# Kernel tuning notes

Hardware: AMD Instinct MI355X
Metric: run time of the kernel (lower is better)

Reference implementation:

```python
import jax, jax.numpy as jnp
import numpy as np

N = 100000      # nodes
E = 1600000     # edges
G = 64          # graphs in batch
H = 128         # hidden (== num_features)
L = 4           # num_layers
C = 16          # num_classes
NCAND = 100000  # candidate edges
BN_EPS = 1e-5


def setup_inputs() -> dict:
    key = jax.random.key(0)
    ks = jax.random.split(key, 24)
    s = 0.05
    inp = {}
    inp["x"] = jax.random.normal(ks[0], (N, H), dtype=jnp.float32)
    inp["edge_index"] = jax.random.randint(ks[1], (2, E), 0, N)
    inp["batch"] = jnp.sort(jax.random.randint(ks[2], (N,), 0, G))
    inp["candidate_edges"] = jax.random.randint(ks[3], (2, NCAND), 0, N)
    # GIN conv params, stacked over L layers (all layers are H->H since num_features==hidden)
    inp["cW1"] = jax.random.normal(ks[4], (L, H, H), dtype=jnp.float32) * s
    inp["cb1"] = jnp.zeros((L, H), jnp.float32)
    inp["cW2"] = jax.random.normal(ks[5], (L, H, H), dtype=jnp.float32) * s
    inp["cb2"] = jnp.zeros((L, H), jnp.float32)
    inp["cgamma"] = jnp.ones((L, H), jnp.float32)
    inp["cbeta"] = jnp.zeros((L, H), jnp.float32)
    inp["ceps"] = jnp.zeros((L,), jnp.float32)  # train_eps=True, init 0
    # node classifier: L*H -> 2H -> H -> H -> C (dropout is identity in eval)
    inp["ncW1"] = jax.random.normal(ks[6], (L * H, 2 * H), dtype=jnp.float32) * s
    inp["ncb1"] = jnp.zeros((2 * H,), jnp.float32)
    inp["ncW2"] = jax.random.normal(ks[7], (2 * H, H), dtype=jnp.float32) * s
    inp["ncb2"] = jnp.zeros((H,), jnp.float32)
    inp["ncW3"] = jax.random.normal(ks[8], (H, H), dtype=jnp.float32) * s
    inp["ncb3"] = jnp.zeros((H,), jnp.float32)
    inp["ncW4"] = jax.random.normal(ks[9], (H, C), dtype=jnp.float32) * s
    inp["ncb4"] = jnp.zeros((C,), jnp.float32)
    # edge predictor: 2*L*H -> 2H -> H -> 1
    inp["epW1"] = jax.random.normal(ks[10], (2 * L * H, 2 * H), dtype=jnp.float32) * s
    inp["epb1"] = jnp.zeros((2 * H,), jnp.float32)
    inp["epW2"] = jax.random.normal(ks[11], (2 * H, H), dtype=jnp.float32) * s
    inp["epb2"] = jnp.zeros((H,), jnp.float32)
    inp["epW3"] = jax.random.normal(ks[12], (H, 1), dtype=jnp.float32) * s
    inp["epb3"] = jnp.zeros((1,), jnp.float32)
    return inp


def _forward(x, cW1, cb1, cW2, cb2, cgamma, cbeta, ceps,
             ncW1, ncb1, ncW2, ncb2, ncW3, ncb3, ncW4, ncb4,
             epW1, epb1, epW2, epb2, epW3, epb3,
             edge_index, batch, candidate_edges):
    src, dst = edge_index[0], edge_index[1]
    h = x
    xs = []
    for l in range(L):
        # GIN: (1+eps)*x_i + sum_{j->i} x_j  (scatter-add over destination nodes)
        agg = jax.ops.segment_sum(h[src], dst, num_segments=N)
        z = (1.0 + ceps[l]) * h + agg
        z = jax.nn.relu(z @ cW1[l] + cb1[l])
        z = jax.nn.relu(z @ cW2[l] + cb2[l])
        # BatchNorm1d (training-mode batch statistics, biased variance)
        mu = z.mean(axis=0)
        var = jnp.var(z, axis=0)
        h = (z - mu) * jax.lax.rsqrt(var + BN_EPS) * cgamma[l] + cbeta[l]
        xs.append(h)
    emb = jnp.concatenate(xs, axis=-1)  # [N, L*H]
    # global mean pool over graphs
    sums = jax.ops.segment_sum(emb, batch, num_segments=G)
    cnt = jax.ops.segment_sum(jnp.ones((N, 1), emb.dtype), batch, num_segments=G)
    gemb = sums / jnp.maximum(cnt, 1.0)  # [G, L*H]
    t = jax.nn.relu(gemb @ ncW1 + ncb1)
    t = jax.nn.relu(t @ ncW2 + ncb2)
    t = jax.nn.relu(t @ ncW3 + ncb3)
    class_output = jax.nn.log_softmax(t @ ncW4 + ncb4, axis=1)  # [G, C]
    # link prediction: gather node embeddings per candidate edge
    ef = jnp.concatenate([emb[candidate_edges[0]], emb[candidate_edges[1]]], axis=1)  # [NC, 2*L*H]
    u = jax.nn.relu(ef @ epW1 + epb1)
    u = jax.nn.relu(u @ epW2 + epb2)
    edge_scores = jax.nn.sigmoid((u @ epW3 + epb3).squeeze(-1))  # [NC]
    return class_output, edge_scores


def reference(x, cW1, cb1, cW2, cb2, cgamma, cbeta, ceps,
              ncW1, ncb1, ncW2, ncb2, ncW3, ncb3, ncW4, ncb4,
              epW1, epb1, epW2, epb2, epW3, epb3,
              edge_index, batch, candidate_edges):
    return _forward(x, cW1, cb1, cW2, cb2, cgamma, cbeta, ceps,
                    ncW1, ncb1, ncW2, ncb2, ncW3, ncb3, ncW4, ncb4,
                    epW1, epb1, epW2, epb2, epW3, epb3,
                    edge_index, batch, candidate_edges)
```

## Files before the change

### kernel.cpp

```cpp
#include <hip/hip_runtime.h>
#include <math.h>

#define NN 100000
#define EE 1600000
#define GG 64
#define HH 128
#define LL 4
#define CCLS 16
#define NC 100000
#define NB 49
#define LDK 40
#define LDA2 136
#define LDC 260

typedef __attribute__((ext_vector_type(8))) short bf16x8;
typedef __attribute__((ext_vector_type(4))) float f32x4;

__device__ __forceinline__ unsigned short f2bf(float x) {
  union { float f; unsigned int u; } v; v.f = x;
  unsigned int r = v.u + 0x7fffu + ((v.u >> 16) & 1u);
  return (unsigned short)(r >> 16);
}
__device__ __forceinline__ float bl(unsigned u) {
  union { unsigned u; float f; } v; v.u = u << 16; return v.f;
}
__device__ __forceinline__ float bh(unsigned u) {
  union { unsigned u; float f; } v; v.u = u & 0xffff0000u; return v.f;
}

__global__ void hist_kernel(const int* __restrict__ dst, int* __restrict__ cnt, int E) {
  int i = (blockIdx.x * 256 + threadIdx.x) * 4;
  if (i + 3 < E) {
    int4 v = *(const int4*)(dst + i);
    atomicAdd(&cnt[v.x], 1);
    atomicAdd(&cnt[v.y], 1);
    atomicAdd(&cnt[v.z], 1);
    atomicAdd(&cnt[v.w], 1);
  } else {
    for (int k = i; k < E; ++k) atomicAdd(&cnt[dst[k]], 1);
  }
}

__global__ __launch_bounds__(256) void scan_p1(const int* __restrict__ cnt,
                                               int* __restrict__ bsum, int n) {
  __shared__ int red[256];
  int tid = threadIdx.x;
  int base = blockIdx.x * 1024 + tid * 4;
  int s = 0;
  if (base + 3 < n) {
    int4 v = *(const int4*)(cnt + base);
    s = v.x + v.y + v.z + v.w;
  } else {
    for (int i = 0; i < 4; ++i) if (base + i < n) s += cnt[base + i];
  }
  red[tid] = s;
  __syncthreads();
  for (int st = 128; st >= 1; st >>= 1) {
    if (tid < st) red[tid] += red[tid + st];
    __syncthreads();
  }
  if (tid == 0) bsum[blockIdx.x] = red[0];
}

__global__ void scan_p2(int* __restrict__ bsum, int* __restrict__ rowptr,
                        int* __restrict__ bcursor, int nb, int n) {
  __shared__ int buf[128];
  int tid = threadIdx.x;
  int v = (tid < nb) ? bsum[tid] : 0;
  buf[tid] = v;
  __syncthreads();
  for (int off = 1; off < 128; off <<= 1) {
    int t = (tid >= off) ? buf[tid - off] : 0;
    __syncthreads();
    buf[tid] += t;
    __syncthreads();
  }
  if (tid < nb) bsum[tid] = buf[tid] - v;
  if (tid == 127) rowptr[n] = buf[127];
  __syncthreads();
  if (tid < NB) bcursor[tid] = bsum[2 * tid];
}

__global__ __launch_bounds__(256) void scan_p3(const int* __restrict__ cnt,
                                               const int* __restrict__ bsum,
                                               int* __restrict__ rowptr,
                                               int* __restrict__ cursor, int n) {
  __shared__ int red[256];
  int tid = threadIdx.x;
  int base = blockIdx.x * 1024 + tid * 4;
  int v[4] = {0, 0, 0, 0};
  if (base + 3 < n) {
    int4 t = *(const int4*)(cnt + base);
    v[0] = t.x; v[1] = t.y; v[2] = t.z; v[3] = t.w;
  } else {
    for (int i = 0; i < 4; ++i) if (base + i < n) v[i] = cnt[base + i];
  }
  int s = v[0] + v[1] + v[2] + v[3];
  red[tid] = s;
  __syncthreads();
  for (int off = 1; off < 256; off <<= 1) {
    int t = (tid >= off) ? red[tid - off] : 0;
    __syncthreads();
    red[tid] += t;
    __syncthreads();
  }
  int run = bsum[blockIdx.x] + red[tid] - s;
  int4 o;
  o.x = run; o.y = run + v[0]; o.z = o.y + v[1]; o.w = o.z + v[2];
  if (base + 3 < n) {
    *(int4*)(rowptr + base) = o;
    *(int4*)(cursor + base) = o;
  } else {
    int oo[4] = {o.x, o.y, o.z, o.w};
    for (int i = 0; i < 4; ++i)
      if (base + i < n) { rowptr[base + i] = oo[i]; cursor[base + i] = oo[i]; }
  }
}

__global__ __launch_bounds__(256) void partition_kernel(const int* __restrict__ src,
                                                        const int* __restrict__ dst,
                                                        int* __restrict__ bcursor,
                                                        int2* __restrict__ pairs, int E) {
  __shared__ int sS[4096];
  __shared__ int sD[4096];
  __shared__ int hist[NB];
  __shared__ int base[NB];
  int tid = threadIdx.x;
  int base_e = blockIdx.x * 4096;
  int cnt = min(4096, E - base_e);
  if (tid < NB) hist[tid] = 0;
  for (int i = tid * 4; i < cnt; i += 1024) {
    if (i + 3 < cnt) {
      *(int4*)(sS + i) = *(const int4*)(src + base_e + i);
      *(int4*)(sD + i) = *(const int4*)(dst + base_e + i);
    } else {
      for (int k = i; k < cnt; ++k) { sS[k] = src[base_e + k]; sD[k] = dst[base_e + k]; }
    }
  }
  __syncthreads();
  for (int i = tid; i < cnt; i += 256) atomicAdd(&hist[sD[i] >> 11], 1);
  __syncthreads();
  if (tid < NB) {
    base[tid] = atomicAdd(&bcursor[tid], hist[tid]);
    hist[tid] = 0;
  }
  __syncthreads();
  for (int i = tid; i < cnt; i += 256) {
    int d = sD[i];
    int b = d >> 11;
    int off = atomicAdd(&hist[b], 1);
    pairs[base[b] + off] = make_int2(sS[i], d);
  }
}

__global__ __launch_bounds__(256) void scatter_csr(const int2* __restrict__ pairs,
                                                   const int* __restrict__ rowptr,
                                                   int* __restrict__ cursor,
                                                   int* __restrict__ csr_src) {
  int b = blockIdx.x % NB;
  int slice = blockIdx.x / NB;
  int start = rowptr[b * 2048];
  int endn = min((b + 1) * 2048, NN);
  int end = rowptr[endn];
  for (int i = start + slice * 256 + threadIdx.x; i < end; i += 8 * 256) {
    int2 p = pairs[i];
    int pos = atomicAdd(&cursor[p.y], 1);
    csr_src[pos] = p.x;
  }
}

#define NF2B (NN * HH / 4)
#define NCVW (LL * 16384 + 32768)
__global__ void convert_all(const float* __restrict__ x, unsigned short* __restrict__ x16,
                            const float* __restrict__ cW1, const float* __restrict__ cW2,
                            unsigned short* __restrict__ WT1, unsigned short* __restrict__ WT2,
                            const float* __restrict__ epW2, unsigned short* __restrict__ W2T) {
  int gi = blockIdx.x * 256 + threadIdx.x;
  if (gi < NF2B) {
    float4 v = ((const float4*)x)[gi];
    unsigned short r[4] = {f2bf(v.x), f2bf(v.y), f2bf(v.z), f2bf(v.w)};
    *(uint2*)(x16 + (size_t)gi * 4) = *(uint2*)r;
    return;
  }
  int idx = gi - NF2B;
  if (idx < LL * 16384) {
    int l = idx >> 14, r = idx & 16383, k = r >> 7, n = r & 127;
    WT1[l * 16384 + n * 128 + k] = f2bf(cW1[idx]);
    WT2[l * 16384 + n * 128 + k] = f2bf(cW2[idx]);
  } else if (idx < NCVW) {
    int j = idx - LL * 16384;
    int k = j >> 7, n = j & 127;
    W2T[(size_t)n * 256 + k] = f2bf(epW2[j]);
  }
}

__global__ __launch_bounds__(256) void ep_w1_prep(
    const float* __restrict__ epW1, const float* __restrict__ epb1,
    const float* __restrict__ bnsum, const float* __restrict__ bnsumsq,
    const float* __restrict__ gamma, const float* __restrict__ beta,
    unsigned short* __restrict__ W1T, float* __restrict__ b1x) {
  __shared__ float red[256];
  int n = blockIdx.x;
  int tid = threadIdx.x;
  const float inv_n = 1.0f / (float)NN;
  int k0 = tid * 4;
  unsigned short w16[4];
  float part = 0.f;
#pragma unroll
  for (int j = 0; j < 4; ++j) {
    int k = k0 + j;
    int c = k & 511;
    float mu = bnsum[c] * inv_n;
    float var = bnsumsq[c] * inv_n - mu * mu;
    float s = rsqrtf(var + 1e-5f) * gamma[c];
    float o = beta[c] - s * mu;
    float w = epW1[(size_t)k * 256 + n];
    w16[j] = f2bf(s * w);
    part += o * w;
  }
  *(uint2*)(W1T + (size_t)n * 1024 + k0) = *(uint2*)w16;
  red[tid] = part;
  __syncthreads();
  for (int st = 128; st >= 1; st >>= 1) {
    if (tid < st) red[tid] += red[tid + st];
    __syncthreads();
  }
  if (tid == 0) b1x[n] = epb1[n] + red[0];
}

__global__ __launch_bounds__(256, 8) void aggregate_bf16(
    const unsigned short* __restrict__ h16, int ld,
    const int* __restrict__ rowptr,
    const int* __restrict__ csr_src,
    const float* __restrict__ ceps_l,
    const float* __restrict__ bnsum_prev,
    const float* __restrict__ bnsumsq_prev,
    const float* __restrict__ gamma_prev,
    const float* __restrict__ beta_prev,
    unsigned short* __restrict__ out, int n) {
  int wave = threadIdx.x >> 6;
  int lane = threadIdx.x & 63;
  int sub = lane >> 4;
  int li = lane & 15;
  int node = blockIdx.x * 16 + wave * 4 + sub;
  if (node >= n) return;
  int c8 = li * 8;
  float acc[8] = {};
  int b = rowptr[node], e = rowptr[node + 1];
  int j = b;
  for (; j + 4 <= e; j += 4) {
    uint4 u[4];
#pragma unroll
    for (int t = 0; t < 4; ++t) {
      int s = csr_src[j + t];
      u[t] = *(const uint4*)(h16 + (size_t)s * ld + c8);
    }
#pragma unroll
    for (int t = 0; t < 4; ++t) {
      acc[0] += bl(u[t].x); acc[1] += bh(u[t].x);
      acc[2] += bl(u[t].y); acc[3] += bh(u[t].y);
      acc[4] += bl(u[t].z); acc[5] += bh(u[t].z);
      acc[6] += bl(u[t].w); acc[7] += bh(u[t].w);
    }
  }
  for (; j < e; ++j) {
    int s = csr_src[j];
    uint4 u = *(const uint4*)(h16 + (size_t)s * ld + c8);
    acc[0] += bl(u.x); acc[1] += bh(u.x);
    acc[2] += bl(u.y); acc[3] += bh(u.y);
    acc[4] += bl(u.z); acc[5] += bh(u.z);
    acc[6] += bl(u.w); acc[7] += bh(u.w);
  }
  float eps1 = 1.0f + *ceps_l;
  uint4 hu = *(const uint4*)(h16 + (size_t)node * ld + c8);
  acc[0] = fmaf(eps1, bl(hu.x), acc[0]); acc[1] = fmaf(eps1, bh(hu.x), acc[1]);
  acc[2] = fmaf(eps1, bl(hu.y), acc[2]); acc[3] = fmaf(eps1, bh(hu.y), acc[3]);
  acc[4] = fmaf(eps1, bl(hu.z), acc[4]); acc[5] = fmaf(eps1, bh(hu.z), acc[5]);
  acc[6] = fmaf(eps1, bl(hu.w), acc[6]); acc[7] = fmaf(eps1, bh(hu.w), acc[7]);
  float degw = (float)(e - b) + eps1;
  unsigned short o[8];
  if (bnsum_prev) {
    const float inv_n = 1.0f / (float)NN;
#pragma unroll
    for (int k = 0; k < 8; ++k) {
      int c = c8 + k;
      float mu = bnsum_prev[c] * inv_n;
      float var = bnsumsq_prev[c] * inv_n - mu * mu;
      float s = rsqrtf(var + 1e-5f) * gamma_prev[c];
      float off = beta_prev[c] - s * mu;
      o[k] = f2bf(fmaf(s, acc[k], degw * off));
    }
  } else {
#pragma unroll
    for (int k = 0; k < 8; ++k) o[k] = f2bf(acc[k]);
  }
  *(uint4*)(out + (size_t)node * 128 + c8) = *(uint4*)o;
}

__global__ __launch_bounds__(256) void trunk_fused(
    const unsigned short* __restrict__ A16,
    const unsigned short* __restrict__ W1T, const float* __restrict__ b1,
    const unsigned short* __restrict__ W2T, const float* __restrict__ b2,
    float* __restrict__ bnsum, float* __restrict__ bnsumsq,
    unsigned short* __restrict__ C16 , int M) {
  __shared__ unsigned short As[128 * LDA2];
  __shared__ unsigned short Bs[128 * LDA2];
  const int tid = threadIdx.x;
  const int bm = blockIdx.x * 128;
  const int lane = tid & 63;
  const int wave = tid >> 6;
  const int wr = (wave >> 1) << 6;
  const int wc = (wave & 1) << 6;
  const int ar = tid >> 1;
  const int ah = (tid & 1) << 4;
  int gra = bm + ar; if (gra >= M) gra = M - 1;
  const unsigned short* Arow = A16 + (size_t)gra * 128;
  const unsigned short* B1row = W1T + (size_t)ar * 128;
  const int mrow = lane & 15;
  const int kq = (lane >> 4) << 3;

  {
    uint4 aR[8], bR[8];
#pragma unroll
    for (int i = 0; i < 4; ++i) {
      aR[2 * i]     = *(const uint4*)(Arow + (i << 5) + ah);
      aR[2 * i + 1] = *(const uint4*)(Arow + (i << 5) + ah + 8);
      bR[2 * i]     = *(const uint4*)(B1row + (i << 5) + ah);
      bR[2 * i + 1] = *(const uint4*)(B1row + (i << 5) + ah + 8);
    }
#pragma unroll
    for (int i = 0; i < 4; ++i) {
      *(uint4*)(As + ar * LDA2 + (i << 5) + ah)     = aR[2 * i];
      *(uint4*)(As + ar * LDA2 + (i << 5) + ah + 8) = aR[2 * i + 1];
      *(uint4*)(Bs + ar * LDA2 + (i << 5) + ah)     = bR[2 * i];
      *(uint4*)(Bs + ar * LDA2 + (i << 5) + ah + 8) = bR[2 * i + 1];
    }
  }
  f32x4 acc[4][4] = {};
  __syncthreads();
#pragma unroll
  for (int ks = 0; ks < 4; ++ks) {
    const int k0 = ks << 5;
    bf16x8 af[4], bfv[4];
#pragma unroll
    for (int t = 0; t < 4; ++t)
      af[t] = *(const bf16x8*)(As + (wr + t * 16 + mrow) * LDA2 + k0 + kq);
#pragma unroll
    for (int t = 0; t < 4; ++t)
      bfv[t] = *(const bf16x8*)(Bs + (wc + t * 16 + mrow) * LDA2 + k0 + kq);
#pragma unroll
    for (int mt = 0; mt < 4; ++mt)
#pragma unroll
      for (int nt = 0; nt < 4; ++nt)
        acc[mt][nt] = __builtin_amdgcn_mfma_f32_16x16x32_bf16(af[mt], bfv[nt], acc[mt][nt], 0, 0, 0);
  }
  uint4 w2[8];
  {
    const unsigned short* B2row = W2T + (size_t)ar * 128;
#pragma unroll
    for (int i = 0; i < 4; ++i) {
      w2[2 * i]     = *(const uint4*)(B2row + (i << 5) + ah);
      w2[2 * i + 1] = *(const uint4*)(B2row + (i << 5) + ah + 8);
    }
  }
  __syncthreads();
  const int crow = (lane >> 4) << 2;
  const int ccol = lane & 15;
#pragma unroll
  for (int nt = 0; nt < 4; ++nt) {
    int c = wc + nt * 16 + ccol;
    float bz = b1[c];
#pragma unroll
    for (int mt = 0; mt < 4; ++mt) {
      int rl = wr + mt * 16 + crow;
#pragma unroll
      for (int i = 0; i < 4; ++i)
        As[(rl + i) * LDA2 + c] = f2bf(fmaxf(acc[mt][nt][i] + bz, 0.f));
    }
  }
#pragma unroll
  for (int i = 0; i < 4; ++i) {
    *(uint4*)(Bs + ar * LDA2 + (i << 5) + ah)     = w2[2 * i];
    *(uint4*)(Bs + ar * LDA2 + (i << 5) + ah + 8) = w2[2 * i + 1];
  }
#pragma unroll
  for (int mt = 0; mt < 4; ++mt)
#pragma unroll
    for (int nt = 0; nt < 4; ++nt)
      acc[mt][nt] = (f32x4){0.f, 0.f, 0.f, 0.f};
  __syncthreads();
#pragma unroll
  for (int ks = 0; ks < 4; ++ks) {
    const int k0 = ks << 5;
    bf16x8 af[4], bfv[4];
#pragma unroll
    for (int t = 0; t < 4; ++t)
      af[t] = *(const bf16x8*)(As + (wr + t * 16 + mrow) * LDA2 + k0 + kq);
#pragma unroll
    for (int t = 0; t < 4; ++t)
      bfv[t] = *(const bf16x8*)(Bs + (wc + t * 16 + mrow) * LDA2 + k0 + kq);
#pragma unroll
    for (int mt = 0; mt < 4; ++mt)
#pragma unroll
      for (int nt = 0; nt < 4; ++nt)
        acc[mt][nt] = __builtin_amdgcn_mfma_f32_16x16x32_bf16(af[mt], bfv[nt], acc[mt][nt], 0, 0, 0);
  }
  __syncthreads();
#pragma unroll
  for (int nt = 0; nt < 4; ++nt) {
    int c = wc + nt * 16 + ccol;
    float bz = b2[c];
    float s = 0.f, q = 0.f;
#pragma unroll
    for (int mt = 0; mt < 4; ++mt) {
      int rl = wr + mt * 16 + crow;
      int rbase = bm + rl;
#pragma unroll
      for (int i = 0; i < 4; ++i) {
        float v = fmaxf(acc[mt][nt][i] + bz, 0.f);
        Bs[(rl + i) * LDA2 + c] = f2bf(v);
        if (rbase + i < M) { s += v; q += v * v; }
      }
    }
    s += __shfl_xor(s, 16, 64);
    s += __shfl_xor(s, 32, 64);
    q += __shfl_xor(q, 16, 64);
    q += __shfl_xor(q, 32, 64);
    if (lane < 16) {
      atomicAdd(&bnsum[c], s);
      atomicAdd(&bnsumsq[c], q);
    }
  }
  __syncthreads();
#pragma unroll
  for (int p = 0; p < 8; ++p) {
    int r = p * 16 + (tid >> 4);
    int q8 = (tid & 15) * 8;
    if (bm + r < M)
      *(uint4*)(C16 + (size_t)(bm + r) * 512 + q8) =
          *(const uint4*)(Bs + r * LDA2 + q8);
  }
}

__global__ __launch_bounds__(512, 4) void ep_fused(
    const unsigned short* __restrict__ emb16, const int* __restrict__ cand,
    const unsigned short* __restrict__ W1T ,
    const float* __restrict__ b1,
    const unsigned short* __restrict__ W2T ,
    const float* __restrict__ b2, const float* __restrict__ epW3,
    const float* __restrict__ epb3,
    float* __restrict__ out, int M) {
  __shared__ unsigned short smem[128 * LDC];
  __shared__ float sDotA[128];
  __shared__ float sDotB[128];
  unsigned short* const As0 = smem;
  unsigned short* const As1 = smem + 128 * LDK;
  unsigned short* const Bs0 = smem + 2 * 128 * LDK;
  unsigned short* const Bs1 = smem + 2 * 128 * LDK + 256 * LDK;
  const int tid = threadIdx.x;
  const int bm = blockIdx.x * 128;
  const int lane = tid & 63;
  const int wave = tid >> 6;
  const int wr = (wave >> 2) << 6;
  const int wc = (wave & 3) << 6;
  f32x4 acc[4][4] = {};
  const int ar = tid >> 2;
  const int ah = (tid & 3) << 3;
  int gra = bm + ar; if (gra >= M) gra = M - 1;
  const int node0 = cand[gra];
  const int node1 = cand[NC + gra];
  const int br = tid >> 1;
  const int bh8 = (tid & 1) << 4;
  const unsigned short* Brow = W1T + (size_t)br * 1024 + bh8;
  const unsigned short* Arow0 = emb16 + (size_t)node0 * 512 + ah;
  const unsigned short* Arow1 = emb16 + (size_t)node1 * 512 + ah - 512;
  const int mrow = lane & 15;
  const int kq = (lane >> 4) << 3;

  auto ldA = [&](int k) -> uint4 {
    const unsigned short* p = (k < 16) ? Arow0 : Arow1;
    return *(const uint4*)(p + (k << 5));
  };
  auto ldB0v = [&](int k) -> uint4 { return *(const uint4*)(Brow + (k << 5)); };
  auto ldB1v = [&](int k) -> uint4 { return *(const uint4*)(Brow + (k << 5) + 8); };
  auto stTile = [&](unsigned short* Ab, unsigned short* Bb, uint4 a, uint4 x0, uint4 x1) {
    *(uint4*)(Ab + ar * LDK + ah) = a;
    *(uint4*)(Bb + br * LDK + bh8) = x0;
    *(uint4*)(Bb + br * LDK + bh8 + 8) = x1;
  };
  auto mma_step = [&](const unsigned short* A, const unsigned short* B) {
    bf16x8 af[4], bfv[4];
#pragma unroll
    for (int t = 0; t < 4; ++t)
      af[t] = *(const bf16x8*)(A + (wr + t * 16 + mrow) * LDK + kq);
#pragma unroll
    for (int t = 0; t < 4; ++t)
      bfv[t] = *(const bf16x8*)(B + (wc + t * 16 + mrow) * LDK + kq);
#pragma unroll
    for (int mt = 0; mt < 4; ++mt)
#pragma unroll
      for (int nt = 0; nt < 4; ++nt)
        acc[mt][nt] = __builtin_amdgcn_mfma_f32_16x16x32_bf16(af[mt], bfv[nt], acc[mt][nt], 0, 0, 0);
  };

  uint4 aA, aB, b0, b1v;
  {
    uint4 a0 = ldA(0), x0 = ldB0v(0), x1 = ldB1v(0);
    stTile(As0, Bs0, a0, x0, x1);
    aA = ldA(1); b0 = ldB0v(1); b1v = ldB1v(1);
    aB = ldA(2);
  }
  __syncthreads();
  for (int it = 0; it < 16; ++it) {
    const int s0 = 2 * it;
    stTile(As1, Bs1, aA, b0, b1v);
    if (s0 + 3 < 32) aA = ldA(s0 + 3);
    if (s0 + 2 < 32) { b0 = ldB0v(s0 + 2); b1v = ldB1v(s0 + 2); }
    mma_step(As0, Bs0);
    __syncthreads();
    const int s1 = s0 + 1;
    if (s1 < 31) {
      stTile(As0, Bs0, aB, b0, b1v);
      if (s1 + 3 < 32) aB = ldA(s1 + 3);
      if (s1 + 2 < 32) { b0 = ldB0v(s1 + 2); b1v = ldB1v(s1 + 2); }
    }
    mma_step(As1, Bs1);
    __syncthreads();
  }

  const int crow = (lane >> 4) << 2;
  const int ccol = lane & 15;
#pragma unroll
  for (int nt = 0; nt < 4; ++nt) {
    int c = wc + nt * 16 + ccol;
    float bz = b1[c];
#pragma unroll
    for (int mt = 0; mt < 4; ++mt) {
      int rl = wr + mt * 16 + crow;
#pragma unroll
      for (int i = 0; i < 4; ++i)
        smem[(rl + i) * LDC + c] = f2bf(fmaxf(acc[mt][nt][i] + bz, 0.f));
    }
  }
  __syncthreads();
  const int wr2 = (wave >> 1) << 5;
  const int wc2 = (wave & 1) << 6;
  f32x4 acc2[2][4] = {};
  for (int ks = 0; ks < 8; ++ks) {
    const int k0 = ks << 5;
    bf16x8 af[2], bfv[4];
#pragma unroll
    for (int t = 0; t < 2; ++t)
      af[t] = *(const bf16x8*)(smem + (wr2 + t * 16 + mrow) * LDC + k0 + kq);
#pragma unroll
    for (int t = 0; t < 4; ++t)
      bfv[t] = *(const bf16x8*)(W2T + (size_t)(wc2 + t * 16 + mrow) * 256 + k0 + kq);
#pragma unroll
    for (int mt = 0; mt < 2; ++mt)
#pragma unroll
      for (int nt = 0; nt < 4; ++nt)
        acc2[mt][nt] = __builtin_amdgcn_mfma_f32_16x16x32_bf16(af[mt], bfv[nt], acc2[mt][nt], 0, 0, 0);
  }
  float w3v[4], bz2[4];
#pragma unroll
  for (int nt = 0; nt < 4; ++nt) {
    int c = wc2 + nt * 16 + ccol;
    w3v[nt] = epW3[c];
    bz2[nt] = b2[c];
  }
  float* sBank = (wave & 1) ? sDotB : sDotA;
#pragma unroll
  for (int mt = 0; mt < 2; ++mt) {
#pragma unroll
    for (int i = 0; i < 4; ++i) {
      int rl = wr2 + mt * 16 + crow + i;
      float p = 0.f;
#pragma unroll
      for (int nt = 0; nt < 4; ++nt)
        p = fmaf(fmaxf(acc2[mt][nt][i] + bz2[nt], 0.f), w3v[nt], p);
      p += __shfl_xor(p, 1, 64);
      p += __shfl_xor(p, 2, 64);
      p += __shfl_xor(p, 4, 64);
      p += __shfl_xor(p, 8, 64);
      if ((lane & 15) == 0) sBank[rl] = p;
    }
  }
  __syncthreads();
  if (tid < 128) {
    int r = bm + tid;
    if (r < M) out[r] = 1.f / (1.f + expf(-(sDotA[tid] + sDotB[tid] + epb3[0])));
  }
}

__global__ __launch_bounds__(256) void pool_bf16(const unsigned short* __restrict__ emb16,
                                                 const int* __restrict__ batch,
                                                 float* __restrict__ gsum) {
  __shared__ int se[2];
  __shared__ float sRed[512];
  int g = blockIdx.x;
  int chunk = blockIdx.y;
  int tid = threadIdx.x;
  if (tid < 2) {
    int x = g + tid;
    int lo = 0, hi = NN;
    while (lo < hi) {
      int mid = (lo + hi) >> 1;
      if (batch[mid] < x) lo = mid + 1; else hi = mid;
    }
    se[tid] = lo;
  }
  __syncthreads();
  int s = se[0], e = se[1];
  int len = e - s;
  int per = (len + 7) >> 3;
  int r0 = s + chunk * per;
  int r1 = min(r0 + per, e);
  int c8 = (tid & 63) * 8;
  int wgrp = tid >> 6;
  float acc[8] = {};
  for (int r = r0 + wgrp; r < r1; r += 4) {
    uint4 u = *(const uint4*)(emb16 + (size_t)r * 512 + c8);
    acc[0] += bl(u.x); acc[1] += bh(u.x);
    acc[2] += bl(u.y); acc[3] += bh(u.y);
    acc[4] += bl(u.z); acc[5] += bh(u.z);
    acc[6] += bl(u.w); acc[7] += bh(u.w);
  }
  if (wgrp == 0) {
#pragma unroll
    for (int j = 0; j < 8; ++j) sRed[c8 + j] = acc[j];
  }
  __syncthreads();
  for (int w = 1; w < 4; ++w) {
    if (wgrp == w) {
#pragma unroll
      for (int j = 0; j < 8; ++j) sRed[c8 + j] += acc[j];
    }
    __syncthreads();
  }
  if (r0 < r1 && tid < 128) {
#pragma unroll
    for (int j = 0; j < 4; ++j)
      atomicAdd(&gsum[g * 512 + tid * 4 + j], sRed[tid * 4 + j]);
  }
}

__global__ __launch_bounds__(256) void nc_fused(
    const float* __restrict__ gsum, const int* __restrict__ batch,
    const float* __restrict__ bnsum, const float* __restrict__ bnsumsq,
    const float* __restrict__ gamma, const float* __restrict__ beta,
    const float* __restrict__ W1, const float* __restrict__ b1,
    const float* __restrict__ W2, const float* __restrict__ b2,
    const float* __restrict__ W3, const float* __restrict__ b3,
    const float* __restrict__ W4, const float* __restrict__ b4,
    float* __restrict__ out) {
  __shared__ float row[512];
  __shared__ float t1[256];
  __shared__ float t2[128];
  __shared__ float t3s[128];
  __shared__ float lg[16];
  __shared__ int se[2];
  int g = blockIdx.x;
  int tid = threadIdx.x;
  if (tid < 2) {
    int x = g + tid;
    int lo = 0, hi = NN;
    while (lo < hi) {
      int mid = (lo + hi) >> 1;
      if (batch[mid] < x) lo = mid + 1; else hi = mid;
    }
    se[tid] = lo;
  }
  __syncthreads();
  float inv = 1.0f / fmaxf((float)(se[1] - se[0]), 1.0f);
  const float inv_n = 1.0f / (float)NN;
#pragma unroll
  for (int h = 0; h < 2; ++h) {
    int c = tid + h * 256;
    float mu = bnsum[c] * inv_n;
    float var = bnsumsq[c] * inv_n - mu * mu;
    float s = rsqrtf(var + 1e-5f) * gamma[c];
    float o = beta[c] - s * mu;
    row[c] = fmaf(gsum[g * 512 + c] * inv, s, o);
  }
  __syncthreads();
  {
    float acc = b1[tid];
#pragma unroll 8
    for (int k = 0; k < 512; ++k) acc = fmaf(row[k], W1[k * 256 + tid], acc);
    t1[tid] = fmaxf(acc, 0.f);
  }
  __syncthreads();
  if (tid < 128) {
    float acc = b2[tid];
#pragma unroll 8
    for (int k = 0; k < 256; ++k) acc = fmaf(t1[k], W2[k * 128 + tid], acc);
    t2[tid] = fmaxf(acc, 0.f);
  }
  __syncthreads();
  if (tid < 128) {
    float acc = b3[tid];
#pragma unroll 8
    for (int k = 0; k < 128; ++k) acc = fmaf(t2[k], W3[k * 128 + tid], acc);
    t3s[tid] = fmaxf(acc, 0.f);
  }
  __syncthreads();
  if (tid < 16) {
    float acc = b4[tid];
#pragma unroll 8
    for (int k = 0; k < 128; ++k) acc = fmaf(t3s[k], W4[k * 16 + tid], acc);
    lg[tid] = acc;
  }
  __syncthreads();
  if (tid < 16) {
    float v = lg[tid];
    float m = v;
    for (int j = 0; j < 16; ++j) m = fmaxf(m, lg[j]);
    float s = 0.f;
    for (int j = 0; j < 16; ++j) s += expf(lg[j] - m);
    out[g * 16 + tid] = v - m - logf(s);
  }
}

extern "C" void kernel_launch(void* const* d_in, const int* in_sizes, int n_in,
                              void* d_out, int out_size, void* d_ws, size_t ws_size,
                              hipStream_t stream) {
  const float* x = (const float*)d_in[0];
  const int* edge_index = (const int*)d_in[1];
  const int* batch = (const int*)d_in[2];
  const int* cand = (const int*)d_in[3];
  const float* cW1 = (const float*)d_in[4];
  const float* cb1 = (const float*)d_in[5];
  const float* cW2 = (const float*)d_in[6];
  const float* cb2 = (const float*)d_in[7];
  const float* cgamma = (const float*)d_in[8];
  const float* cbeta = (const float*)d_in[9];
  const float* ceps = (const float*)d_in[10];
  const float* ncW1 = (const float*)d_in[11];
  const float* ncb1 = (const float*)d_in[12];
  const float* ncW2 = (const float*)d_in[13];
  const float* ncb2 = (const float*)d_in[14];
  const float* ncW3 = (const float*)d_in[15];
  const float* ncb3 = (const float*)d_in[16];
  const float* ncW4 = (const float*)d_in[17];
  const float* ncb4 = (const float*)d_in[18];
  const float* epW1 = (const float*)d_in[19];
  const float* epb1 = (const float*)d_in[20];
  const float* epW2 = (const float*)d_in[21];
  const float* epb2 = (const float*)d_in[22];
  const float* epW3 = (const float*)d_in[23];
  const float* epb3 = (const float*)d_in[24];

  char* ws = (char*)d_ws;
  size_t off = 0;
  auto alloc = [&](size_t bytes) -> void* {
    off = (off + 255) & ~(size_t)255;
    void* p = ws + off;
    off += bytes;
    return p;
  };
  size_t zz_bytes = (size_t)NN * 4 + 512 * 4 + 512 * 4 + (size_t)GG * 512 * 4;
  char* zz = (char*)alloc(zz_bytes);
  int* cnt = (int*)zz;
  float* bnsum = (float*)(zz + (size_t)NN * 4);
  float* bnsumsq = bnsum + 512;
  float* gsum = bnsumsq + 512;
  int* rowptr = (int*)alloc((size_t)(NN + 1) * 4);
  int* cursor = (int*)alloc((size_t)NN * 4);
  int* csr_src = (int*)alloc((size_t)EE * 4);
  int2* pairs = (int2*)alloc((size_t)EE * 8);
  int* bsum = (int*)alloc(128 * 4);
  int* bcursor = (int*)alloc(64 * 4);
  unsigned short* x16 = (unsigned short*)alloc((size_t)NN * 128 * 2);
  unsigned short* g16a = (unsigned short*)alloc((size_t)NN * 128 * 2);
  unsigned short* emb16 = (unsigned short*)alloc((size_t)NN * 512 * 2);
  unsigned short* WT1 = (unsigned short*)alloc((size_t)LL * 16384 * 2);
  unsigned short* WT2 = (unsigned short*)alloc((size_t)LL * 16384 * 2);
  unsigned short* W1T = (unsigned short*)alloc((size_t)1024 * 256 * 2);
  unsigned short* W2T = (unsigned short*)alloc((size_t)256 * 128 * 2);
  float* b1x = (float*)alloc(256 * 4);

  const int* esrc = edge_index;
  const int* edst = edge_index + EE;
  const int nblk = (NN + 1023) / 1024;
  const int nech = (EE + 4095) / 4096;

  hipMemsetAsync(zz, 0, zz_bytes, stream);
  hist_kernel<<<(EE / 4 + 255) / 256, 256, 0, stream>>>(edst, cnt, EE);
  scan_p1<<<nblk, 256, 0, stream>>>(cnt, bsum, NN);
  scan_p2<<<1, 128, 0, stream>>>(bsum, rowptr, bcursor, nblk, NN);
  scan_p3<<<nblk, 256, 0, stream>>>(cnt, bsum, rowptr, cursor, NN);
  partition_kernel<<<nech, 256, 0, stream>>>(esrc, edst, bcursor, pairs, EE);
  scatter_csr<<<NB * 8, 256, 0, stream>>>(pairs, rowptr, cursor, csr_src);
  convert_all<<<(NF2B + NCVW + 255) / 256, 256, 0, stream>>>(
      x, x16, cW1, cW2, WT1, WT2, epW2, W2T);

  for (int l = 0; l < LL; ++l) {
    const unsigned short* h16 = (l == 0) ? x16 : (emb16 + (size_t)(l - 1) * 128);
    int ld = (l == 0) ? 128 : 512;
    aggregate_bf16<<<(NN + 15) / 16, 256, 0, stream>>>(
        h16, ld, rowptr, csr_src, ceps + l,
        (l == 0) ? nullptr : bnsum + (l - 1) * 128,
        (l == 0) ? nullptr : bnsumsq + (l - 1) * 128,
        (l == 0) ? nullptr : cgamma + (l - 1) * 128,
        (l == 0) ? nullptr : cbeta + (l - 1) * 128,
        g16a, NN);
    trunk_fused<<<(NN + 127) / 128, 256, 0, stream>>>(
        g16a, WT1 + (size_t)l * 16384, cb1 + l * 128,
        WT2 + (size_t)l * 16384, cb2 + l * 128,
        bnsum + l * 128, bnsumsq + l * 128, emb16 + (size_t)l * 128, NN);
  }
  ep_w1_prep<<<256, 256, 0, stream>>>(epW1, epb1, bnsum, bnsumsq, cgamma, cbeta,
                                      W1T, b1x);

  pool_bf16<<<dim3(GG, 8), 256, 0, stream>>>(emb16, batch, gsum);
  nc_fused<<<GG, 256, 0, stream>>>(gsum, batch, bnsum, bnsumsq, cgamma, cbeta,
                                   ncW1, ncb1, ncW2, ncb2, ncW3, ncb3,
                                   ncW4, ncb4, (float*)d_out);

  ep_fused<<<(NC + 127) / 128, 512, 0, stream>>>(
      emb16, cand, W1T, b1x, W2T, epb2, epW3, epb3,
      (float*)d_out + GG * CCLS, NC);
}
```

Baseline: 1.002 ms.

## Use finer 256-node buckets and LDS-local sort to build CSR

Edge partitioning now uses 391 buckets of 256 destination nodes instead of 49 buckets of 2048, and the CSR scatter sorts each bucket inside shared memory with per-node offsets in LDS. Each bucket's sorted sources are then written back contiguously. This removes the global cursor array and the global atomics with scattered writes in the final CSR pass. In exchange there are more buckets, so more global atomics on bcursor per partition block, plus a fallback path when a bucket exceeds the shared-memory capacity.

```diff
diff --git a/kernel.cpp b/kernel.cpp
--- a/kernel.cpp
+++ b/kernel.cpp
@@ -8,7 +8,8 @@
 #define LL 4
 #define CCLS 16
 #define NC 100000
-#define NB 49
+#define NB2 391
+#define SCAP 6144
 #define LDK 40
 #define LDA2 136
 #define LDC 260
@@ -62,8 +63,7 @@
   if (tid == 0) bsum[blockIdx.x] = red[0];
 }
 
-__global__ void scan_p2(int* __restrict__ bsum, int* __restrict__ rowptr,
-                        int* __restrict__ bcursor, int nb, int n) {
+__global__ void scan_p2(int* __restrict__ bsum, int* __restrict__ rowptr, int nb, int n) {
   __shared__ int buf[128];
   int tid = threadIdx.x;
   int v = (tid < nb) ? bsum[tid] : 0;
@@ -77,14 +77,11 @@
   }
   if (tid < nb) bsum[tid] = buf[tid] - v;
   if (tid == 127) rowptr[n] = buf[127];
-  __syncthreads();
-  if (tid < NB) bcursor[tid] = bsum[2 * tid];
 }
 
 __global__ __launch_bounds__(256) void scan_p3(const int* __restrict__ cnt,
                                                const int* __restrict__ bsum,
-                                               int* __restrict__ rowptr,
-                                               int* __restrict__ cursor, int n) {
+                                               int* __restrict__ rowptr, int n) {
   __shared__ int red[256];
   int tid = threadIdx.x;
   int base = blockIdx.x * 1024 + tid * 4;
@@ -109,12 +106,16 @@
   o.x = run; o.y = run + v[0]; o.z = o.y + v[1]; o.w = o.z + v[2];
   if (base + 3 < n) {
     *(int4*)(rowptr + base) = o;
-    *(int4*)(cursor + base) = o;
   } else {
     int oo[4] = {o.x, o.y, o.z, o.w};
     for (int i = 0; i < 4; ++i)
-      if (base + i < n) { rowptr[base + i] = oo[i]; cursor[base + i] = oo[i]; }
-  }
+      if (base + i < n) rowptr[base + i] = oo[i];
+  }
+}
+
+__global__ void bcursor_init(const int* __restrict__ rowptr, int* __restrict__ bcursor) {
+  int b = blockIdx.x * 256 + threadIdx.x;
+  if (b < NB2) bcursor[b] = rowptr[b * 256];
 }
 
 __global__ __launch_bounds__(256) void partition_kernel(const int* __restrict__ src,
@@ -123,12 +124,12 @@
                                                         int2* __restrict__ pairs, int E) {
   __shared__ int sS[4096];
   __shared__ int sD[4096];
-  __shared__ int hist[NB];
-  __shared__ int base[NB];
+  __shared__ int hist[NB2 + 1];
+  __shared__ int base[NB2 + 1];
   int tid = threadIdx.x;
   int base_e = blockIdx.x * 4096;
   int cnt = min(4096, E - base_e);
-  if (tid < NB) hist[tid] = 0;
+  for (int h = tid; h < NB2; h += 256) hist[h] = 0;
   for (int i = tid * 4; i < cnt; i += 1024) {
     if (i + 3 < cnt) {
       *(int4*)(sS + i) = *(const int4*)(src + base_e + i);
@@ -138,34 +139,48 @@
     }
   }
   __syncthreads();
-  for (int i = tid; i < cnt; i += 256) atomicAdd(&hist[sD[i] >> 11], 1);
-  __syncthreads();
-  if (tid < NB) {
-    base[tid] = atomicAdd(&bcursor[tid], hist[tid]);
-    hist[tid] = 0;
+  for (int i = tid; i < cnt; i += 256) atomicAdd(&hist[sD[i] >> 8], 1);
+  __syncthreads();
+  for (int h = tid; h < NB2; h += 256) {
+    base[h] = atomicAdd(&bcursor[h], hist[h]);
+    hist[h] = 0;
   }
   __syncthreads();
   for (int i = tid; i < cnt; i += 256) {
     int d = sD[i];
-    int b = d >> 11;
+    int b = d >> 8;
     int off = atomicAdd(&hist[b], 1);
     pairs[base[b] + off] = make_int2(sS[i], d);
   }
 }
 
-__global__ __launch_bounds__(256) void scatter_csr(const int2* __restrict__ pairs,
-                                                   const int* __restrict__ rowptr,
-                                                   int* __restrict__ cursor,
-                                                   int* __restrict__ csr_src) {
-  int b = blockIdx.x % NB;
-  int slice = blockIdx.x / NB;
-  int start = rowptr[b * 2048];
-  int endn = min((b + 1) * 2048, NN);
-  int end = rowptr[endn];
-  for (int i = start + slice * 256 + threadIdx.x; i < end; i += 8 * 256) {
-    int2 p = pairs[i];
-    int pos = atomicAdd(&cursor[p.y], 1);
-    csr_src[pos] = p.x;
+__global__ __launch_bounds__(256) void scatter_sort(const int2* __restrict__ pairs,
+                                                    const int* __restrict__ rowptr,
+                                                    int* __restrict__ csr_src) {
+  __shared__ int lofs[256];
+  __shared__ int sbuf[SCAP];
+  int b = blockIdx.x;
+  int tid = threadIdx.x;
+  int n0 = b * 256;
+  int nodes = min(256, NN - n0);
+  int pstart = rowptr[n0];
+  int L = rowptr[n0 + nodes] - pstart;
+  if (tid < nodes) lofs[tid] = rowptr[n0 + tid] - pstart;
+  __syncthreads();
+  if (L <= SCAP) {
+    for (int i = tid; i < L; i += 256) {
+      int2 p = pairs[pstart + i];
+      int pos = atomicAdd(&lofs[p.y - n0], 1);
+      sbuf[pos] = p.x;
+    }
+    __syncthreads();
+    for (int i = tid; i < L; i += 256) csr_src[pstart + i] = sbuf[i];
+  } else {
+    for (int i = tid; i < L; i += 256) {
+      int2 p = pairs[pstart + i];
+      int pos = atomicAdd(&lofs[p.y - n0], 1);
+      csr_src[pstart + pos] = p.x;
+    }
   }
 }
 
@@ -765,11 +780,10 @@
   float* bnsumsq = bnsum + 512;
   float* gsum = bnsumsq + 512;
   int* rowptr = (int*)alloc((size_t)(NN + 1) * 4);
-  int* cursor = (int*)alloc((size_t)NN * 4);
   int* csr_src = (int*)alloc((size_t)EE * 4);
   int2* pairs = (int2*)alloc((size_t)EE * 8);
   int* bsum = (int*)alloc(128 * 4);
-  int* bcursor = (int*)alloc(64 * 4);
+  int* bcursor = (int*)alloc(512 * 4);
   unsigned short* x16 = (unsigned short*)alloc((size_t)NN * 128 * 2);
   unsigned short* g16a = (unsigned short*)alloc((size_t)NN * 128 * 2);
   unsigned short* emb16 = (unsigned short*)alloc((size_t)NN * 512 * 2);
@@ -787,10 +801,11 @@
   hipMemsetAsync(zz, 0, zz_bytes, stream);
   hist_kernel<<<(EE / 4 + 255) / 256, 256, 0, stream>>>(edst, cnt, EE);
   scan_p1<<<nblk, 256, 0, stream>>>(cnt, bsum, NN);
-  scan_p2<<<1, 128, 0, stream>>>(bsum, rowptr, bcursor, nblk, NN);
-  scan_p3<<<nblk, 256, 0, stream>>>(cnt, bsum, rowptr, cursor, NN);
+  scan_p2<<<1, 128, 0, stream>>>(bsum, rowptr, nblk, NN);
+  scan_p3<<<nblk, 256, 0, stream>>>(cnt, bsum, rowptr, NN);
+  bcursor_init<<<(NB2 + 255) / 256, 256, 0, stream>>>(rowptr, bcursor);
   partition_kernel<<<nech, 256, 0, stream>>>(esrc, edst, bcursor, pairs, EE);
-  scatter_csr<<<NB * 8, 256, 0, stream>>>(pairs, rowptr, cursor, csr_src);
+  scatter_sort<<<NB2, 256, 0, stream>>>(pairs, rowptr, csr_src);
   convert_all<<<(NF2B + NCVW + 255) / 256, 256, 0, stream>>>(
       x, x16, cW1, cW2, WT1, WT2, epW2, W2T);
 
```

New measurement: 910.2 us. 1.1x faster.
